# Optimization experiments

Measured on AMD Instinct MI355X. Metric: run time of the kernel, lower is better.

## Reference

```python
import jax, jax.numpy as jnp
import numpy as np

GROUP_SIZES = [5, 5, 5, 5, 5, 5, 4]  # 7 concept groups, sum = 34
LN_EPS = 1e-5


def setup_inputs() -> dict:
    key = jax.random.key(0)
    ks = jax.random.split(key, 12)
    B, N, D, K, P, C, NC, H = 256, 196, 768, 7, 512, 34, 7, 3072
    img_feat_map = jax.random.normal(ks[0], (B, N, D), dtype=jnp.float32)
    # torch: Embedding weight uniform in [-1/K, 1/K]
    vq_codebook = (jax.random.uniform(ks[1], (K, D), dtype=jnp.float32) * 2.0 - 1.0) / K
    agg_codebook = jax.random.normal(ks[2], (K, D), dtype=jnp.float32)
    W1 = jax.random.normal(ks[3], (D, H), dtype=jnp.float32) * 0.02
    b1 = jnp.zeros((H,), dtype=jnp.float32)
    W2 = jax.random.normal(ks[4], (H, D), dtype=jnp.float32) * 0.02
    b2 = jnp.zeros((D,), dtype=jnp.float32)
    ln_gamma = jnp.ones((D,), dtype=jnp.float32)
    ln_beta = jnp.zeros((D,), dtype=jnp.float32)
    W_proj = jax.random.normal(ks[5], (D, P), dtype=jnp.float32) * 0.02
    concept_emb = jax.random.normal(ks[6], (C, P), dtype=jnp.float32)
    concept_emb = concept_emb / jnp.linalg.norm(concept_emb, axis=-1, keepdims=True)
    cls_W = jax.random.normal(ks[7], (C, NC), dtype=jnp.float32) * 0.02
    cls_b = jnp.zeros((NC,), dtype=jnp.float32)
    logit_scale = jnp.float32(100.0)  # detached CLIP logit scale
    return {
        "img_feat_map": img_feat_map, "vq_codebook": vq_codebook,
        "agg_codebook": agg_codebook, "W1": W1, "b1": b1, "W2": W2, "b2": b2,
        "ln_gamma": ln_gamma, "ln_beta": ln_beta, "W_proj": W_proj,
        "concept_emb": concept_emb, "cls_W": cls_W, "cls_b": cls_b,
        "logit_scale": logit_scale,
    }


def _pairwise_sq_dists(x, cb):
    # x: [B, N, D], cb: [K, D] -> [B, N, K]
    x_sq = jnp.sum(x * x, axis=-1, keepdims=True)           # [B, N, 1]
    cb_sq = jnp.sum(cb * cb, axis=-1)                        # [K]
    dot = jnp.einsum("bnd,kd->bnk", x, cb)                  # [B, N, K]
    return x_sq + cb_sq - 2.0 * dot


def _avg_effective_rank(x, threshold=0.99):
    # x: [B, N, D]; per-sample SVD, rank = #{cumsum(S)/sum(S) <= thr}
    S = jnp.linalg.svd(jax.lax.stop_gradient(x), compute_uv=False)  # [B, min(N,D)]
    energy = jnp.cumsum(S, axis=-1) / jnp.sum(S, axis=-1, keepdims=True)
    ranks = jnp.sum(energy <= threshold, axis=-1)
    return jnp.mean(ranks.astype(jnp.float32))


def reference(img_feat_map, vq_codebook, agg_codebook, W1, b1, W2, b2,
              ln_gamma, ln_beta, W_proj, concept_emb, cls_W, cls_b, logit_scale):
    x = img_feat_map  # [B, N, D]

    avg_rank = _avg_effective_rank(x)

    # --- VectorQuantizeAggregator: soft assignment to 7 codes ---
    d_agg = _pairwise_sq_dists(x, agg_codebook)              # [B, N, K]
    soft = jax.nn.softmax(-d_agg, axis=-1)                   # [B, N, K]
    agg = jnp.einsum("bnk,bnd->bkd", soft, x)               # [B, K, D]

    # --- VectorQuantizer: hard argmin + gather (one-hot @ codebook) ---
    d_vq = _pairwise_sq_dists(x, vq_codebook)                # [B, N, K]
    idx = jnp.argmin(d_vq, axis=-1)                          # [B, N] int
    quantized = vq_codebook[idx]                             # [B, N, D] gather == onehot @ cb
    sg = jax.lax.stop_gradient
    codebook_loss = jnp.mean((quantized - sg(x)) ** 2)
    commitment_loss = jnp.mean((sg(quantized) - x) ** 2)
    vq_loss = codebook_loss + 1.0 * commitment_loss

    # --- bridge: FFN -> LayerNorm -> proj -> L2 normalize ---
    h = jax.nn.gelu(agg @ W1 + b1, approximate=False) @ W2 + b2  # [B, K, D]
    mu = jnp.mean(h, axis=-1, keepdims=True)
    var = jnp.mean((h - mu) ** 2, axis=-1, keepdims=True)
    hn = (h - mu) * jax.lax.rsqrt(var + LN_EPS) * ln_gamma + ln_beta
    tok = hn @ W_proj                                        # [B, K, 512]
    tok = tok / jnp.linalg.norm(tok, axis=-1, keepdims=True)

    # --- per-group concept logits: token g vs its concept slice ---
    logits_list = []
    start = 0
    for g, sz in enumerate(GROUP_SIZES):
        ce = concept_emb[start:start + sz]                   # [sz, 512]
        logits_list.append(logit_scale * (tok[:, g, :] @ ce.T))  # [B, sz]
        start += sz
    image_logits = jnp.concatenate(logits_list, axis=-1)     # [B, 34]

    cls_logits = image_logits @ cls_W + cls_b                # [B, 7]
    return (cls_logits, image_logits, vq_loss, avg_rank)
```

## Files before the change

### kernel.cpp

```cpp
#include <hip/hip_runtime.h>
#include <hip/hip_bf16.h>
#include <math.h>

using hbf = __hip_bfloat16;
typedef __bf16 bf16x8 __attribute__((ext_vector_type(8)));
typedef float f32x4 __attribute__((ext_vector_type(4)));

__device__ inline float r16d(float v){
  int x;
  x = __builtin_bit_cast(int, v);
  v += __builtin_bit_cast(float, __builtin_amdgcn_mov_dpp(x, 0x121, 0xf, 0xf, true));
  x = __builtin_bit_cast(int, v);
  v += __builtin_bit_cast(float, __builtin_amdgcn_mov_dpp(x, 0x122, 0xf, 0xf, true));
  x = __builtin_bit_cast(int, v);
  v += __builtin_bit_cast(float, __builtin_amdgcn_mov_dpp(x, 0x124, 0xf, 0xf, true));
  x = __builtin_bit_cast(int, v);
  v += __builtin_bit_cast(float, __builtin_amdgcn_mov_dpp(x, 0x128, 0xf, 0xf, true));
  return v;
}
__device__ inline void r16d4(float& a, float& b, float& c, float& d){
#define R16STAGE(ctl) { \
  int xa=__builtin_bit_cast(int,a), xb=__builtin_bit_cast(int,b); \
  int xc=__builtin_bit_cast(int,c), xd=__builtin_bit_cast(int,d); \
  a += __builtin_bit_cast(float, __builtin_amdgcn_mov_dpp(xa, ctl, 0xf, 0xf, true)); \
// ... 99 lines not shown
    }
    cx0 = nx0; cx1 = nx1; cx2 = nx2;
  }
  __syncthreads();
  for (int i = tid; i < 5376; i += 512) cA[i] = 0.f;
  __syncthreads();
  for (int w = 0; w < 8; ++w){
    if (wave == w){
#pragma unroll
      for (int k = 0; k < 7; ++k)
#pragma unroll
        for (int c = 0; c < 3; ++c){
          float* p = &cA[k*768 + c*256 + (lane<<2)];
          p[0] += aR[k][c].x; p[1] += aR[k][c].y; p[2] += aR[k][c].z; p[3] += aR[k][c].w;
        }
    }
    __syncthreads();
  }
  for (int i = tid; i < 5376; i += 512) aggbf[(size_t)b*5376 + i] = __float2bfloat16(cA[i]);
  if (lane == 0) atomicAdd(&scal[0], loss);
}

__global__ __launch_bounds__(512) void k_gram(const float* __restrict__ x, float* __restrict__ G){
  __shared__ hbf Xs[208*104];
  const int tid = threadIdx.x, lane = tid & 63, wave = tid >> 6;
  const int b = blockIdx.x;
  const int l15 = lane & 15;
  const int fr0 = wave, fr1 = wave + 8;
  const bool f1 = (fr1 < 13);
  f32x4 acc0[13] = {};
  f32x4 acc1[13] = {};
  const float* xb = x + (size_t)b*196*768;
  for (int kc = 0; kc < 8; ++kc){
    __syncthreads();
    for (int u = tid; u < 4992; u += 512){
      const int r = u / 24, c4 = u - r*24;
      ushort4 val;
      if (r < 196){
        float4 f = *(const float4*)(xb + (size_t)r*768 + kc*96 + c4*4);
        hbf t0 = __float2bfloat16(f.x), t1 = __float2bfloat16(f.y);
        hbf t2 = __float2bfloat16(f.z), t3 = __float2bfloat16(f.w);
        val.x = *(const unsigned short*)&t0; val.y = *(const unsigned short*)&t1;
        val.z = *(const unsigned short*)&t2; val.w = *(const unsigned short*)&t3;
      } else { val.x = 0; val.y = 0; val.z = 0; val.w = 0; }
      *(ushort4*)&Xs[r*104 + c4*4] = val;
    }
    __syncthreads();
#pragma unroll
    for (int kk = 0; kk < 3; ++kk){
      const int ko = kk*32 + (lane>>4)*8;
      bf16x8 a0 = *(const bf16x8*)&Xs[(fr0*16 + l15)*104 + ko];
      bf16x8 a1 = f1 ? *(const bf16x8*)&Xs[(fr1*16 + l15)*104 + ko] : a0;
#pragma unroll
      for (int fc = 0; fc < 13; ++fc){
        bf16x8 bb = *(const bf16x8*)&Xs[(fc*16 + l15)*104 + ko];
        acc0[fc] = __builtin_amdgcn_mfma_f32_16x16x32_bf16(a0, bb, acc0[fc], 0, 0, 0);
        if (f1) acc1[fc] = __builtin_amdgcn_mfma_f32_16x16x32_bf16(a1, bb, acc1[fc], 0, 0, 0);
      }
    }
  }
  const size_t gb = (size_t)b*38416;
  const int cr = (lane>>4)*4;
#pragma unroll
  for (int fc = 0; fc < 13; ++fc){
    const int gc = fc*16 + l15;
    if (gc < 196){
#pragma unroll
      for (int r = 0; r < 4; ++r){
        const int gr = fr0*16 + cr + r;
        if (gr < 196) G[gb + (size_t)gr*196 + gc] = acc0[fc][r];
      }
      if (f1){
#pragma unroll
        for (int r = 0; r < 4; ++r){
          const int gr = fr1*16 + cr + r;
          if (gr < 196) G[gb + (size_t)gr*196 + gc] = acc1[fc][r];
        }
      }
    }
  }
}

#define ESTR 196
#define FOLD4(vv4) { vv4.x = (oc==0)? v0 : vv4.x; vv4.y = (oc==1)? v0 : vv4.y; \
                     vv4.z = (oc==2)? v0 : vv4.z; vv4.w = (oc==3)? v0 : vv4.w; }
#define VHOIST(colc, out) { \
  const int col_ = (colc) + jc4; \
  const float4 xv_ = *(const float4*)(rowk + col_); \
  float4 vp_; \
  if (col_ > base){ vp_ = xv_; } \
  else if (col_ + 3 <= base){ vp_ = make_float4(0.f,0.f,0.f,0.f); } \
  else { vp_.x = 0.f; \
         vp_.y = (col_+1 > base) ? xv_.y : 0.f; \
         vp_.z = (col_+2 > base) ? xv_.z : 0.f; \
         vp_.w = xv_.w; } \
  out = vp_; sig += vp_.x*vp_.x + vp_.y*vp_.y + vp_.z*vp_.z + vp_.w*vp_.w; }

__global__ __launch_bounds__(1024) void k_eigen(const float* __restrict__ G, float* __restrict__ scal){
  extern __shared__ float S[];
  float* A   = S;
  float* ww  = S + 38496;
  float* dd  = S + 38752;
  float* ee  = S + 38952;
  float* e2  = S + 39152;
  float* red2= S + 39352;
  const int n = 196;
  const int tid = threadIdx.x, lane = tid & 63, wave = tid >> 6;
  const int grp = lane >> 4, c16 = lane & 15;
  const int jc4 = c16 << 2;
  const int rbase = (wave << 2) + grp;
  const int b = blockIdx.x;
  {
    const float4* Gv = (const float4*)(G + (size_t)b*38416);
    float4* Av = (float4*)A;
    for (int u = tid; u < 9604; u += 1024) Av[u] = Gv[u];
    if (tid < 80) S[38416 + tid] = 0.f;
    if (tid < 256) ww[tid] = 0.f;
  }
  __syncthreads();
  for (int k = 0; k <= 130; ++k){
    const int base = k + 1, m = n - 1 - k;
    const float* rowk = &A[(size_t)k*ESTR];
    const float x0 = rowk[base];
    if (tid == 0) ww[k] = 0.f;
    float4 v4_0, v4_1, v4_2, v4_3;
    float sig = 0.f;
    VHOIST(0,   v4_0)
    VHOIST(64,  v4_1)
    VHOIST(128, v4_2)
    {
      float4 vp_ = make_float4(0.f,0.f,0.f,0.f);
      if (c16 == 0){
        vp_ = *(const float4*)(rowk + 192);
        sig += vp_.x*vp_.x + vp_.y*vp_.y + vp_.z*vp_.z + vp_.w*vp_.w;
      }
      v4_3 = vp_;
    }
    sig = r16d(sig);
    float tau = 0.f, v0 = 0.f, alpha = x0;
    if (sig > 1e-20f){
      const float mu = sqrtf(x0*x0 + sig);
      alpha = (x0 > 0.f) ? -mu : mu;
      v0 = x0 - alpha;
      tau = 2.f/(sig + v0*v0);
    }
    if (tid == 0) ee[k] = alpha;
    if (c16 == ((base >> 2) & 15)){
      const int oc = base & 3;
      const int op = base >> 6;
      if (op == 0){ FOLD4(v4_0) } else if (op == 1){ FOLD4(v4_1) } else { FOLD4(v4_2) }
    }
    const int p0 = base >> 6;
    const int i0 = rbase, i1 = 64 + rbase, i2 = 128 + rbase, i3 = 192 + rbase;
    float vr_0=0.f, vr_1=0.f, vr_2=0.f, vr_3=0.f;
    float wr_0=0.f, wr_1=0.f, wr_2=0.f, wr_3=0.f;
    if (tau != 0.f){
      float a0c=0.f, a1c=0.f, a2c=0.f, a3c=0.f;
#define MV_T(IV, ACC) { \
      if (IV < m){ \
        const float* Ar = &A[(size_t)(base+IV)*ESTR]; \
        if (0 >= p0){ ACC += d4(*(const float4*)(Ar + jc4),       v4_0); } \
        if (1 >= p0){ ACC += d4(*(const float4*)(Ar + 64 + jc4),  v4_1); } \
        if (2 >= p0){ ACC += d4(*(const float4*)(Ar + 128 + jc4), v4_2); } \
        if (c16 == 0){ ACC += d4(*(const float4*)(Ar + 192), v4_3); } } }
      MV_T(i0, a0c)
      MV_T(i1, a1c)
      MV_T(i2, a2c)
      MV_T(i3, a3c)
#undef MV_T
      r16d4(a0c, a1c, a2c, a3c);
      float cpart = 0.f;
      {
        wr_0 = tau*a0c;
        vr_0 = (i0 == 0) ? v0 : rowk[base+i0];
        cpart += vr_0*wr_0;
        if (c16 == 0) ww[base+i0] = wr_0;
      }
      if (i1 < m){
        wr_1 = tau*a1c; vr_1 = rowk[base+i1];
        cpart += vr_1*wr_1;
        if (c16 == 0) ww[base+i1] = wr_1;
      }
      if (i2 < m){
        wr_2 = tau*a2c; vr_2 = rowk[base+i2];
        cpart += vr_2*wr_2;
        if (c16 == 0) ww[base+i2] = wr_2;
      }
      if (i3 < m){
        wr_3 = tau*a3c; vr_3 = rowk[base+i3];
        cpart += vr_3*wr_3;
        if (c16 == 0) ww[base+i3] = wr_3;
      }
      cpart += __shfl_xor(cpart, 16);
      cpart += __shfl_xor(cpart, 32);
      if (lane == 0) red2[wave] = cpart;
    }
    __syncthreads();
    if (tau != 0.f){
      const float4* r2 = (const float4*)red2;
      const float4 q0 = r2[0], q1 = r2[1], q2 = r2[2], q3 = r2[3];
      const float vtw = (q0.x+q0.y+q0.z+q0.w) + (q1.x+q1.y+q1.z+q1.w)
                      + (q2.x+q2.y+q2.z+q2.w) + (q3.x+q3.y+q3.z+q3.w);
      const float c2 = 0.5f*tau*vtw;
      float4 w4_0, w4_1, w4_2, w4_3 = make_float4(0.f,0.f,0.f,0.f);
      { const float4 t4 = *(const float4*)(ww + jc4);
        w4_0.x = t4.x - c2*v4_0.x; w4_0.y = t4.y - c2*v4_0.y; w4_0.z = t4.z - c2*v4_0.z; w4_0.w = t4.w - c2*v4_0.w; }
      { const float4 t4 = *(const float4*)(ww + 64 + jc4);
        w4_1.x = t4.x - c2*v4_1.x; w4_1.y = t4.y - c2*v4_1.y; w4_1.z = t4.z - c2*v4_1.z; w4_1.w = t4.w - c2*v4_1.w; }
      { const float4 t4 = *(const float4*)(ww + 128 + jc4);
        w4_2.x = t4.x - c2*v4_2.x; w4_2.y = t4.y - c2*v4_2.y; w4_2.z = t4.z - c2*v4_2.z; w4_2.w = t4.w - c2*v4_2.w; }
      if (c16 == 0){
        const float4 t4 = *(const float4*)(ww + 192);
        w4_3.x = t4.x - c2*v4_3.x; w4_3.y = t4.y - c2*v4_3.y; w4_3.z = t4.z - c2*v4_3.z; w4_3.w = t4.w - c2*v4_3.w; }
#define UP_T(IV, VRV, WRV) { \
      if (IV < m){ \
        const float vi = VRV; \
        const float wi = WRV - c2*vi; \
        float* Ar = &A[(size_t)(base+IV)*ESTR]; \
        if (0 >= p0){ float4 a = *(const float4*)(Ar + jc4); \
          a.x -= vi*w4_0.x + wi*v4_0.x; a.y -= vi*w4_0.y + wi*v4_0.y; \
          a.z -= vi*w4_0.z + wi*v4_0.z; a.w -= vi*w4_0.w + wi*v4_0.w; \
          *(float4*)(Ar + jc4) = a; } \
        if (1 >= p0){ float4 a = *(const float4*)(Ar + 64 + jc4); \
          a.x -= vi*w4_1.x + wi*v4_1.x; a.y -= vi*w4_1.y + wi*v4_1.y; \
          a.z -= vi*w4_1.z + wi*v4_1.z; a.w -= vi*w4_1.w + wi*v4_1.w; \
          *(float4*)(Ar + 64 + jc4) = a; } \
        if (2 >= p0){ float4 a = *(const float4*)(Ar + 128 + jc4); \
          a.x -= vi*w4_2.x + wi*v4_2.x; a.y -= vi*w4_2.y + wi*v4_2.y; \
          a.z -= vi*w4_2.z + wi*v4_2.z; a.w -= vi*w4_2.w + wi*v4_2.w; \
          *(float4*)(Ar + 128 + jc4) = a; } \
        if (c16 == 0){ float4 a = *(const float4*)(Ar + 192); \
          a.x -= vi*w4_3.x + wi*v4_3.x; a.y -= vi*w4_3.y + wi*v4_3.y; \
          a.z -= vi*w4_3.z + wi*v4_3.z; a.w -= vi*w4_3.w + wi*v4_3.w; \
          *(float4*)(Ar + 192) = a; } } }
      UP_T(i0, vr_0, wr_0)
      UP_T(i1, vr_1, wr_1)
      UP_T(i2, vr_2, wr_2)
      UP_T(i3, vr_3, wr_3)
#undef UP_T
    }
    __syncthreads();
  }
  if (wave == 0){
    float vrT[16], wrT[16];
    for (int k = 131; k <= n-3; ++k){
      const int base = k + 1, m = n - 1 - k;
      const float* rowk = &A[(size_t)k*ESTR];
      const float x0 = rowk[base];
      if (lane == 0) ww[k] = 0.f;
      float4 v4_2, v4_3;
      float sig = 0.f;
      VHOIST(128, v4_2)
      {
        float4 vp_ = make_float4(0.f,0.f,0.f,0.f);
        if (c16 == 0){
          const float4 xv_ = *(const float4*)(rowk + 192);
          if (192 > base){ vp_ = xv_; }
          else { vp_.x = 0.f;
                 vp_.y = (193 > base) ? xv_.y : 0.f;
                 vp_.z = (194 > base) ? xv_.z : 0.f;
                 vp_.w = xv_.w; }
        }
        v4_3 = vp_; sig += vp_.x*vp_.x + vp_.y*vp_.y + vp_.z*vp_.z + vp_.w*vp_.w;
      }
      sig = r16d(sig);
      float tau = 0.f, v0 = 0.f, alpha = x0;
      if (sig > 1e-20f){
        const float mu = sqrtf(x0*x0 + sig);
        alpha = (x0 > 0.f) ? -mu : mu;
        v0 = x0 - alpha;
        tau = 2.f/(sig + v0*v0);
      }
      if (lane == 0) ee[k] = alpha;
      if (c16 == ((base >> 2) & 15)){
        const int oc = base & 3;
        if ((base >> 6) == 2){ FOLD4(v4_2) } else { FOLD4(v4_3) }
      }
      if (tau != 0.f){
        float cpart = 0.f;
#pragma unroll
        for (int t = 0; t < 16; ++t){
          const int i_ = (t << 2) + grp;
          float vrv = 0.f, wrv = 0.f;
          if (i_ < m){
            const float* Ar = &A[(size_t)(base+i_)*ESTR];
            float acc = d4(*(const float4*)(Ar + 128 + jc4), v4_2);
            if (c16 == 0) acc += d4(*(const float4*)(Ar + 192), v4_3);
            acc = r16d(acc);
            wrv = tau*acc;
            vrv = (i_ == 0) ? v0 : rowk[base+i_];
            cpart += vrv*wrv;
            if (c16 == 0) ww[base+i_] = wrv;
          }
          vrT[t] = vrv; wrT[t] = wrv;
        }
        cpart += __shfl_xor(cpart, 16);
        cpart += __shfl_xor(cpart, 32);
        const float c2 = 0.5f*tau*cpart;
        __threadfence_block();
        float4 w4_2, w4_3 = make_float4(0.f,0.f,0.f,0.f);
        { const float4 t4 = *(const float4*)(ww + 128 + jc4);
          w4_2.x = t4.x - c2*v4_2.x; w4_2.y = t4.y - c2*v4_2.y; w4_2.z = t4.z - c2*v4_2.z; w4_2.w = t4.w - c2*v4_2.w; }
        if (c16 == 0){
          const float4 t4 = *(const float4*)(ww + 192);
          w4_3.x = t4.x - c2*v4_3.x; w4_3.y = t4.y - c2*v4_3.y; w4_3.z = t4.z - c2*v4_3.z; w4_3.w = t4.w - c2*v4_3.w; }
#pragma unroll
        for (int t = 0; t < 16; ++t){
          const int i_ = (t << 2) + grp;
          if (i_ < m){
            const float vi = vrT[t];
            const float wi = wrT[t] - c2*vi;
            float* Ar = &A[(size_t)(base+i_)*ESTR];
            float4 a = *(const float4*)(Ar + 128 + jc4);
            a.x -= vi*w4_2.x + wi*v4_2.x; a.y -= vi*w4_2.y + wi*v4_2.y;
            a.z -= vi*w4_2.z + wi*v4_2.z; a.w -= vi*w4_2.w + wi*v4_2.w;
            *(float4*)(Ar + 128 + jc4) = a;
            if (c16 == 0){
              float4 a3 = *(const float4*)(Ar + 192);
              a3.x -= vi*w4_3.x + wi*v4_3.x; a3.y -= vi*w4_3.y + wi*v4_3.y;
              a3.z -= vi*w4_3.z + wi*v4_3.z; a3.w -= vi*w4_3.w + wi*v4_3.w;
              *(float4*)(Ar + 192) = a3;
            }
          }
        }
        __threadfence_block();
      }
    }
  }
  __syncthreads();
  if (tid < n) dd[tid] = A[(size_t)tid*ESTR + tid];
  if (tid == 0) ee[n-2] = A[(size_t)(n-1)*ESTR + (n-2)];
  __syncthreads();
  if (tid < n-1) e2[tid] = ee[tid]*ee[tid];
  __syncthreads();
  float lo = 1e30f, hi = -1e30f;
  if (tid < n){
    const float rr = ((tid > 0) ? fabsf(ee[tid-1]) : 0.f) + ((tid < n-1) ? fabsf(ee[tid]) : 0.f);
    lo = dd[tid] - rr; hi = dd[tid] + rr;
  }
  {
    float l2 = lo, h2 = hi;
#pragma unroll
    for (int o = 32; o > 0; o >>= 1){
      l2 = fminf(l2, __shfl_xor(l2, o));
      h2 = fmaxf(h2, __shfl_xor(h2, o));
    }
    if (lane == 0){ ww[wave] = l2; red2[wave] = h2; }
  }
  __syncthreads();
  float glo = ww[0], ghi = red2[0];
#pragma unroll
  for (int w2 = 1; w2 < 16; ++w2){ glo = fminf(glo, ww[w2]); ghi = fmaxf(ghi, red2[w2]); }
  __syncthreads();
  float sv = 0.f;
  if (tid < n){
    float lob = glo, hib = ghi;
    for (int it2 = 0; it2 < 18; ++it2){
      const float mid = 0.5f*(lob + hib);
      float q = dd[0] - mid;
      int cnt = (q < 0.f) ? 1 : 0;
      for (int i = 1; i < n; ++i){
        const float r = fast_rcp(q);
        q = (dd[i] - mid) - e2[i-1]*r;
        q = (fabsf(q) < 1e-6f) ? -1e-6f : q;
        cnt += (q < 0.f) ? 1 : 0;
      }
      if (cnt <= tid) lob = mid; else hib = mid;
    }
    sv = sqrtf(fmaxf(0.5f*(lob + hib), 0.f));
  }
  __syncthreads();
  if (tid < n) ww[tid] = sv;
  __syncthreads();
  if (tid == 0){
    float tot = 0.f;
    for (int i = 0; i < n; ++i) tot += ww[i];
    const float thr = 0.99f*tot;
    float cs = 0.f; int rank = 0;
    for (int i = n-1; i >= 0; --i){ cs += ww[i]; rank += (cs <= thr) ? 1 : 0; }
    atomicAdd(&scal[1], (float)rank);
  }
}

__global__ __launch_bounds__(256) void k_tr(const float* __restrict__ in, hbf* __restrict__ outp,
                                            int Rr, int Cc){
  __shared__ float t[32][33];
  const int tid = threadIdx.x;
  const int lc = tid & 31, lr = tid >> 5;
  const int c0 = blockIdx.x*32, r0 = blockIdx.y*32;
#pragma unroll
  for (int i = 0; i < 4; ++i)
    t[lr + i*8][lc] = in[(size_t)(r0 + lr + i*8)*Cc + c0 + lc];
  __syncthreads();
#pragma unroll
  for (int i = 0; i < 4; ++i)
    outp[(size_t)(c0 + lr + i*8)*Rr + r0 + lc] = __float2bfloat16(t[lc][lr + i*8]);
}

template<int EPI>
__global__ __launch_bounds__(512) void k_gemm128(const hbf* __restrict__ Aa, const hbf* __restrict__ Bb,
    const float* __restrict__ bias, void* __restrict__ outp, int Ni, int Ki){
  __shared__ hbf As[128*72];
  __shared__ hbf Bs[128*72];
  const int tid = threadIdx.x, lane = tid & 63, wave = tid >> 6;
  const int row0 = blockIdx.y*128, col0 = blockIdx.x*128;
  const int m0 = (wave >> 2)*64, n0 = (wave & 3)*32;
  const int l15 = lane & 15, lk = (lane >> 4)*8;
  const int sr = tid >> 3, sc = (tid & 7)*8;
  f32x4 acc[4][2] = {};
  for (int kt = 0; kt < Ki; kt += 64){
    __syncthreads();
    *(uint4*)&As[sr*72 + sc]      = *(const uint4*)&Aa[(size_t)(row0+sr)*Ki + kt + sc];
    *(uint4*)&As[(sr+64)*72 + sc] = *(const uint4*)&Aa[(size_t)(row0+sr+64)*Ki + kt + sc];
    *(uint4*)&Bs[sr*72 + sc]      = *(const uint4*)&Bb[(size_t)(col0+sr)*Ki + kt + sc];
    *(uint4*)&Bs[(sr+64)*72 + sc] = *(const uint4*)&Bb[(size_t)(col0+sr+64)*Ki + kt + sc];
    __syncthreads();
#pragma unroll
    for (int kk = 0; kk < 2; ++kk){
      const int ko = kk*32 + lk;
      bf16x8 b0 = *(const bf16x8*)&Bs[(n0 + l15)*72 + ko];
      bf16x8 b1 = *(const bf16x8*)&Bs[(n0 + 16 + l15)*72 + ko];
#pragma unroll
      for (int mi = 0; mi < 4; ++mi){
        bf16x8 a = *(const bf16x8*)&As[(m0 + mi*16 + l15)*72 + ko];
        acc[mi][0] = __builtin_amdgcn_mfma_f32_16x16x32_bf16(a, b0, acc[mi][0], 0, 0, 0);
        acc[mi][1] = __builtin_amdgcn_mfma_f32_16x16x32_bf16(a, b1, acc[mi][1], 0, 0, 0);
      }
    }
  }
  const int cr = (lane >> 4)*4;
#pragma unroll
  for (int mi = 0; mi < 4; ++mi){
#pragma unroll
    for (int ni = 0; ni < 2; ++ni){
      const int gcol = col0 + n0 + ni*16 + l15;
#pragma unroll
      for (int r = 0; r < 4; ++r){
        const int grow = row0 + m0 + mi*16 + cr + r;
        float v = acc[mi][ni][r];
        if (EPI == 1){
          v += bias[gcol];
          v = 0.5f*v*(1.f + erff(v*0.70710678118654752f));
          ((hbf*)outp)[(size_t)grow*Ni + gcol] = __float2bfloat16(v);
        } else if (EPI == 2){
          v += bias[gcol];
          ((float*)outp)[(size_t)grow*Ni + gcol] = v;
        } else {
          ((float*)outp)[(size_t)grow*Ni + gcol] = v;
        }
      }
    }
  }
}

template<int EPI>
__global__ __launch_bounds__(256) void k_gemm(const hbf* __restrict__ Aa, const hbf* __restrict__ Bb,
    const float* __restrict__ bias, void* __restrict__ outp, int Mi, int Ni, int Ki){
  __shared__ hbf As[64*72];
  __shared__ hbf Bs[64*72];
  const int tid = threadIdx.x, lane = tid & 63, wave = tid >> 6;
  const int row0 = blockIdx.y*64, col0 = blockIdx.x*64;
  const int m0 = (wave >> 1)*32, n0 = (wave & 1)*32;
// ... 84 lines not shown
__global__ __launch_bounds__(256) void k_head(const float* __restrict__ tok, const float* __restrict__ ce,
    const float* __restrict__ clsW, const float* __restrict__ clsb, const float* __restrict__ lgs,
    float* __restrict__ out){
  __shared__ float tkn[7*512];
  __shared__ float il[40];
  const int tid = threadIdx.x, lane = tid & 63, wave = tid >> 6;
  const int b = blockIdx.x;
  const float ls = lgs[0];
  for (int g = wave; g < 7; g += 4){
    const float* tr = tok + (size_t)(b*7 + g)*512;
    float4 u0 = *(const float4*)(tr + (lane<<3));
    float4 u1 = *(const float4*)(tr + (lane<<3) + 4);
    float s = d4(u0,u0) + d4(u1,u1);
    s = wred(s);
    const float inv = 1.f/sqrtf(s);
    float* dst = &tkn[g*512 + (lane<<3)];
    dst[0] = u0.x*inv; dst[1] = u0.y*inv; dst[2] = u0.z*inv; dst[3] = u0.w*inv;
    dst[4] = u1.x*inv; dst[5] = u1.y*inv; dst[6] = u1.z*inv; dst[7] = u1.w*inv;
  }
  __syncthreads();
  for (int c = wave; c < 34; c += 4){
    const int g = (c < 30) ? (c/5) : 6;
    const float* tp = &tkn[g*512 + (lane<<3)];
    const float* cp = ce + (size_t)c*512 + (lane<<3);
    float s = tp[0]*cp[0] + tp[1]*cp[1] + tp[2]*cp[2] + tp[3]*cp[3]
            + tp[4]*cp[4] + tp[5]*cp[5] + tp[6]*cp[6] + tp[7]*cp[7];
    s = wred(s);
    if (lane == 0){
      const float v = ls*s;
      il[c] = v;
      out[1792 + b*34 + c] = v;
    }
  }
  __syncthreads();
  if (tid < 7){
    float s = clsb[tid];
    for (int c = 0; c < 34; ++c) s += il[c]*clsW[c*7 + tid];
    out[b*7 + tid] = s;
  }
}

__global__ void k_fin(const float* __restrict__ scal, float* __restrict__ out){
  if (threadIdx.x == 0){
    out[10496] = 2.f*scal[0]/(float)(256*196*768);
    out[10497] = scal[1]*(1.f/256.f);
  }
}

extern "C" void kernel_launch(void* const* d_in, const int* in_sizes, int n_in,
                              void* d_out, int out_size, void* d_ws, size_t ws_size,
                              hipStream_t stream) {
  (void)in_sizes; (void)n_in; (void)out_size; (void)ws_size;
  const float* x    = (const float*)d_in[0];
  const float* vqcb = (const float*)d_in[1];
  const float* agcb = (const float*)d_in[2];
  const float* W1   = (const float*)d_in[3];
  const float* b1   = (const float*)d_in[4];
  const float* W2   = (const float*)d_in[5];
  const float* b2   = (const float*)d_in[6];
  const float* gam  = (const float*)d_in[7];
  const float* bet  = (const float*)d_in[8];
  const float* Wp   = (const float*)d_in[9];
  const float* ce   = (const float*)d_in[10];
  const float* clsW = (const float*)d_in[11];
  const float* clsb = (const float*)d_in[12];
  const float* lgs  = (const float*)d_in[13];
  float* out = (float*)d_out;
  char* w = (char*)d_ws;

  float* scal  = (float*)w;
  float* G     = (float*)(w + 256);
  hbf*   aggbf = (hbf*)(w + 39338240ULL);
  hbf*   W1t   = (hbf*)(w + 42090752ULL);
  hbf*   W2t   = (hbf*)(w + 46809344ULL);
  hbf*   Wpt   = (hbf*)(w + 51527936ULL);
  hbf*   h1    = (hbf*)(w + 256);
  float* hbuf  = (float*)(w + 256 + 16777216ULL);
  hbf*   hn    = (hbf*)(w + 256 + 25165824ULL);
  float* tok   = (float*)(w + 256 + 29360128ULL);

  k_init<<<dim3(1), dim3(64), 0, stream>>>(scal);
  k_dist<<<dim3(256), dim3(512), 0, stream>>>(x, vqcb, agcb, aggbf, scal);
  k_gram<<<dim3(256), dim3(512), 0, stream>>>(x, G);
  const int EIG_SMEM = 39368*4;
  hipFuncSetAttribute((const void*)k_eigen, hipFuncAttributeMaxDynamicSharedMemorySize, EIG_SMEM);
  k_eigen<<<dim3(256), dim3(1024), EIG_SMEM, stream>>>(G, scal);
  k_tr<<<dim3(96,24), dim3(256), 0, stream>>>(W1, W1t, 768, 3072);
  k_tr<<<dim3(24,96), dim3(256), 0, stream>>>(W2, W2t, 3072, 768);
  k_tr<<<dim3(16,24), dim3(256), 0, stream>>>(Wp, Wpt, 768, 512);
  k_gemm128<1><<<dim3(24,14), dim3(512), 0, stream>>>(aggbf, W1t, b1, (void*)h1, 3072, 768);
  k_gemm<2><<<dim3(12,28), dim3(256), 0, stream>>>(h1, W2t, b2, (void*)hbuf, 1792, 768, 3072);
  k_ln<<<dim3(448), dim3(256), 0, stream>>>(hbuf, gam, bet, hn);
  k_gemm<3><<<dim3(8,28), dim3(256), 0, stream>>>(hn, Wpt, nullptr, (void*)tok, 1792, 512, 768);
  k_head<<<dim3(256), dim3(256), 0, stream>>>(tok, ce, clsW, clsb, lgs, out);
  k_fin<<<dim3(1), dim3(64), 0, stream>>>(scal, out);
}
```

Before: 1.034 ms.

## Block Householder tridiagonalization two reflectors per step in eigen kernel

Restructures the Householder tridiagonalization in k_eigen so each iteration computes two reflectors and applies a combined rank-4 update to the shared-memory matrix. The second reflector's vector and matvec are derived on the fly from the first update without materializing the intermediate matrix. This halves the number of full matrix read-modify-write passes and the associated block barriers per reflector pair. In exchange it adds extra reductions and register pressure, and the serial single-wave tail now starts one step later.

```diff
diff --git a/kernel.cpp b/kernel.cpp
--- a/kernel.cpp
+++ b/kernel.cpp
@@ -205,28 +205,30 @@
 }
 
 #define ESTR 196
-#define FOLD4(vv4) { vv4.x = (oc==0)? v0 : vv4.x; vv4.y = (oc==1)? v0 : vv4.y; \
-                     vv4.z = (oc==2)? v0 : vv4.z; vv4.w = (oc==3)? v0 : vv4.w; }
-#define VHOIST(colc, out) { \
-  const int col_ = (colc) + jc4; \
+#define FOLD4v(FR, V0) { FR.x = (oc==0)? (V0) : FR.x; FR.y = (oc==1)? (V0) : FR.y; \
+                         FR.z = (oc==2)? (V0) : FR.z; FR.w = (oc==3)? (V0) : FR.w; }
+#define VH(COLC, BASE, OUT) { \
+  const int col_ = (COLC) + jc4; \
   const float4 xv_ = *(const float4*)(rowk + col_); \
   float4 vp_; \
-  if (col_ > base){ vp_ = xv_; } \
-  else if (col_ + 3 <= base){ vp_ = make_float4(0.f,0.f,0.f,0.f); } \
+  if (col_ > (BASE)){ vp_ = xv_; } \
+  else if (col_ + 3 <= (BASE)){ vp_ = make_float4(0.f,0.f,0.f,0.f); } \
   else { vp_.x = 0.f; \
-         vp_.y = (col_+1 > base) ? xv_.y : 0.f; \
-         vp_.z = (col_+2 > base) ? xv_.z : 0.f; \
+         vp_.y = (col_+1 > (BASE)) ? xv_.y : 0.f; \
+         vp_.z = (col_+2 > (BASE)) ? xv_.z : 0.f; \
          vp_.w = xv_.w; } \
-  out = vp_; sig += vp_.x*vp_.x + vp_.y*vp_.y + vp_.z*vp_.z + vp_.w*vp_.w; }
+  OUT = vp_; sig += vp_.x*vp_.x + vp_.y*vp_.y + vp_.z*vp_.z + vp_.w*vp_.w; }
 
 __global__ __launch_bounds__(1024) void k_eigen(const float* __restrict__ G, float* __restrict__ scal){
   extern __shared__ float S[];
-  float* A   = S;
-  float* ww  = S + 38496;
-  float* dd  = S + 38752;
-  float* ee  = S + 38952;
-  float* e2  = S + 39152;
-  float* red2= S + 39352;
+  float* A    = S;
+  float* ww1  = S + 38496;
+  float* ww2  = S + 38752;
+  float* dd   = S + 39008;
+  float* ee   = S + 39208;
+  float* e2   = S + 39408;
+  float* red2 = S + 39608;
+  float* red2b= S + 39624;
   const int n = 196;
   const int tid = threadIdx.x, lane = tid & 63, wave = tid >> 6;
   const int grp = lane >> 4, c16 = lane & 15;
@@ -237,143 +239,247 @@
     const float4* Gv = (const float4*)(G + (size_t)b*38416);
     float4* Av = (float4*)A;
     for (int u = tid; u < 9604; u += 1024) Av[u] = Gv[u];
-    if (tid < 80) S[38416 + tid] = 0.f;
-    if (tid < 256) ww[tid] = 0.f;
-  }
-  __syncthreads();
-  for (int k = 0; k <= 130; ++k){
-    const int base = k + 1, m = n - 1 - k;
-    const float* rowk = &A[(size_t)k*ESTR];
-    const float x0 = rowk[base];
-    if (tid == 0) ww[k] = 0.f;
-    float4 v4_0, v4_1, v4_2, v4_3;
+    if (tid < 592) S[38416 + tid] = 0.f;
+  }
+  __syncthreads();
+  for (int k = 0; k <= 130; k += 2){
+    const int base1 = k + 1, base2 = k + 2;
+    const int m1 = n - 1 - k, m2 = n - 2 - k;
+    const float* rowk  = &A[(size_t)k*ESTR];
+    const float* rowk1 = &A[(size_t)base1*ESTR];
+    if (tid == 0 && k > 0){
+      ww1[k-1] = 0.f; ww1[k] = 0.f;
+      ww2[k]   = 0.f; ww2[k+1] = 0.f;
+    }
+    const float x01 = rowk[base1];
+    float4 v1f0, v1f1, v1f2, v1f3;
     float sig = 0.f;
-    VHOIST(0,   v4_0)
-    VHOIST(64,  v4_1)
-    VHOIST(128, v4_2)
+    VH(0,   base1, v1f0)
+    VH(64,  base1, v1f1)
+    VH(128, base1, v1f2)
+    { float4 vp = make_float4(0.f,0.f,0.f,0.f);
+      if (c16 == 0){ vp = *(const float4*)(rowk + 192);
+        sig += vp.x*vp.x + vp.y*vp.y + vp.z*vp.z + vp.w*vp.w; }
+      v1f3 = vp; }
+    sig = r16d(sig);
+    float tau1 = 0.f, v01 = 0.f, alpha1 = x01;
+    if (sig > 1e-20f){
+      const float mu = sqrtf(x01*x01 + sig);
+      alpha1 = (x01 > 0.f) ? -mu : mu;
+      v01 = x01 - alpha1;
+      tau1 = 2.f/(sig + v01*v01);
+    }
+    if (tid == 0) ee[k] = alpha1;
+    if (c16 == ((base1 >> 2) & 15)){
+      const int oc = base1 & 3, op = base1 >> 6;
+      if (op == 0){ FOLD4v(v1f0, v01) } else if (op == 1){ FOLD4v(v1f1, v01) } else { FOLD4v(v1f2, v01) }
+    }
+    const int p0 = base1 >> 6;
+    const int i0r = rbase, i1r = 64 + rbase, i2r = 128 + rbase, i3r = 192 + rbase;
     {
-      float4 vp_ = make_float4(0.f,0.f,0.f,0.f);
-      if (c16 == 0){
-        vp_ = *(const float4*)(rowk + 192);
-        sig += vp_.x*vp_.x + vp_.y*vp_.y + vp_.z*vp_.z + vp_.w*vp_.w;
-      }
-      v4_3 = vp_;
-    }
-    sig = r16d(sig);
-    float tau = 0.f, v0 = 0.f, alpha = x0;
-    if (sig > 1e-20f){
-      const float mu = sqrtf(x0*x0 + sig);
-      alpha = (x0 > 0.f) ? -mu : mu;
-      v0 = x0 - alpha;
-      tau = 2.f/(sig + v0*v0);
-    }
-    if (tid == 0) ee[k] = alpha;
-    if (c16 == ((base >> 2) & 15)){
-      const int oc = base & 3;
-      const int op = base >> 6;
-      if (op == 0){ FOLD4(v4_0) } else if (op == 1){ FOLD4(v4_1) } else { FOLD4(v4_2) }
-    }
-    const int p0 = base >> 6;
-    const int i0 = rbase, i1 = 64 + rbase, i2 = 128 + rbase, i3 = 192 + rbase;
-    float vr_0=0.f, vr_1=0.f, vr_2=0.f, vr_3=0.f;
-    float wr_0=0.f, wr_1=0.f, wr_2=0.f, wr_3=0.f;
-    if (tau != 0.f){
-      float a0c=0.f, a1c=0.f, a2c=0.f, a3c=0.f;
-#define MV_T(IV, ACC) { \
-      if (IV < m){ \
-        const float* Ar = &A[(size_t)(base+IV)*ESTR]; \
-        if (0 >= p0){ ACC += d4(*(const float4*)(Ar + jc4),       v4_0); } \
-        if (1 >= p0){ ACC += d4(*(const float4*)(Ar + 64 + jc4),  v4_1); } \
-        if (2 >= p0){ ACC += d4(*(const float4*)(Ar + 128 + jc4), v4_2); } \
-        if (c16 == 0){ ACC += d4(*(const float4*)(Ar + 192), v4_3); } } }
-      MV_T(i0, a0c)
-      MV_T(i1, a1c)
-      MV_T(i2, a2c)
-      MV_T(i3, a3c)
-#undef MV_T
+      float a0c = 0.f, a1c = 0.f, a2c = 0.f, a3c = 0.f;
+#define MV1(IV, ACC) { \
+      if ((IV) < m1){ \
+        const float* Ar = &A[(size_t)(base1+(IV))*ESTR]; \
+        if (0 >= p0) ACC += d4(*(const float4*)(Ar + jc4), v1f0); \
+        if (1 >= p0) ACC += d4(*(const float4*)(Ar + 64 + jc4), v1f1); \
+        if (2 >= p0) ACC += d4(*(const float4*)(Ar + 128 + jc4), v1f2); \
+        if (c16 == 0) ACC += d4(*(const float4*)(Ar + 192), v1f3); } }
+      MV1(i0r, a0c) MV1(i1r, a1c) MV1(i2r, a2c) MV1(i3r, a3c)
+#undef MV1
       r16d4(a0c, a1c, a2c, a3c);
-      float cpart = 0.f;
-      {
-        wr_0 = tau*a0c;
-        vr_0 = (i0 == 0) ? v0 : rowk[base+i0];
-        cpart += vr_0*wr_0;
-        if (c16 == 0) ww[base+i0] = wr_0;
-      }
-      if (i1 < m){
-        wr_1 = tau*a1c; vr_1 = rowk[base+i1];
-        cpart += vr_1*wr_1;
-        if (c16 == 0) ww[base+i1] = wr_1;
-      }
-      if (i2 < m){
-        wr_2 = tau*a2c; vr_2 = rowk[base+i2];
-        cpart += vr_2*wr_2;
-        if (c16 == 0) ww[base+i2] = wr_2;
-      }
-      if (i3 < m){
-        wr_3 = tau*a3c; vr_3 = rowk[base+i3];
-        cpart += vr_3*wr_3;
-        if (c16 == 0) ww[base+i3] = wr_3;
-      }
-      cpart += __shfl_xor(cpart, 16);
-      cpart += __shfl_xor(cpart, 32);
-      if (lane == 0) red2[wave] = cpart;
-    }
-    __syncthreads();
-    if (tau != 0.f){
+      float cp = 0.f;
+#define CP1(IV, ACC) { \
+      if ((IV) < m1){ \
+        const float wr_ = tau1*(ACC); \
+        const float vr_ = ((IV) == 0) ? v01 : rowk[base1+(IV)]; \
+        cp += vr_*wr_; \
+        if (c16 == 0) ww1[base1+(IV)] = wr_; } }
+      CP1(i0r, a0c) CP1(i1r, a1c) CP1(i2r, a2c) CP1(i3r, a3c)
+#undef CP1
+      cp += __shfl_xor(cp, 16);
+      cp += __shfl_xor(cp, 32);
+      if (lane == 0) red2[wave] = cp;
+    }
+    __syncthreads();
+    float c21, w1head, tau2 = 0.f, v02 = 0.f;
+    float4 w1f0, w1f1, w1f2, w1f3;
+    float4 v2f0, v2f1, v2f2, v2f3;
+    {
       const float4* r2 = (const float4*)red2;
       const float4 q0 = r2[0], q1 = r2[1], q2 = r2[2], q3 = r2[3];
       const float vtw = (q0.x+q0.y+q0.z+q0.w) + (q1.x+q1.y+q1.z+q1.w)
                       + (q2.x+q2.y+q2.z+q2.w) + (q3.x+q3.y+q3.z+q3.w);
-      const float c2 = 0.5f*tau*vtw;
-      float4 w4_0, w4_1, w4_2, w4_3 = make_float4(0.f,0.f,0.f,0.f);
-      { const float4 t4 = *(const float4*)(ww + jc4);
-        w4_0.x = t4.x - c2*v4_0.x; w4_0.y = t4.y - c2*v4_0.y; w4_0.z = t4.z - c2*v4_0.z; w4_0.w = t4.w - c2*v4_0.w; }
-      { const float4 t4 = *(const float4*)(ww + 64 + jc4);
-        w4_1.x = t4.x - c2*v4_1.x; w4_1.y = t4.y - c2*v4_1.y; w4_1.z = t4.z - c2*v4_1.z; w4_1.w = t4.w - c2*v4_1.w; }
-      { const float4 t4 = *(const float4*)(ww + 128 + jc4);
-        w4_2.x = t4.x - c2*v4_2.x; w4_2.y = t4.y - c2*v4_2.y; w4_2.z = t4.z - c2*v4_2.z; w4_2.w = t4.w - c2*v4_2.w; }
-      if (c16 == 0){
-        const float4 t4 = *(const float4*)(ww + 192);
-        w4_3.x = t4.x - c2*v4_3.x; w4_3.y = t4.y - c2*v4_3.y; w4_3.z = t4.z - c2*v4_3.z; w4_3.w = t4.w - c2*v4_3.w; }
-#define UP_T(IV, VRV, WRV) { \
-      if (IV < m){ \
-        const float vi = VRV; \
-        const float wi = WRV - c2*vi; \
-        float* Ar = &A[(size_t)(base+IV)*ESTR]; \
+      c21 = 0.5f*tau1*vtw;
+      w1head = ww1[base1] - c21*v01;
+      if (tid == 0) A[(size_t)base1*ESTR + base1] = rowk1[base1] - 2.f*v01*w1head;
+#define W1F(COLC, VF, OUT) { \
+      const float4 t4 = *(const float4*)(ww1 + (COLC) + jc4); \
+      OUT.x = t4.x - c21*VF.x; OUT.y = t4.y - c21*VF.y; \
+      OUT.z = t4.z - c21*VF.z; OUT.w = t4.w - c21*VF.w; }
+      W1F(0,   v1f0, w1f0)
+      W1F(64,  v1f1, w1f1)
+      W1F(128, v1f2, w1f2)
+      { float4 wp = make_float4(0.f,0.f,0.f,0.f);
+        if (c16 == 0){ const float4 t4 = *(const float4*)(ww1 + 192);
+          wp.x = t4.x - c21*v1f3.x; wp.y = t4.y - c21*v1f3.y;
+          wp.z = t4.z - c21*v1f3.z; wp.w = t4.w - c21*v1f3.w; }
+        w1f3 = wp; }
+#undef W1F
+      float sig2 = 0.f;
+#define V2F(COLC, VF1, WF1, OUT) { \
+      const int col_ = (COLC) + jc4; \
+      const float4 r1_ = *(const float4*)(rowk1 + col_); \
+      float4 rp_; \
+      rp_.x = r1_.x - v01*WF1.x - w1head*VF1.x; \
+      rp_.y = r1_.y - v01*WF1.y - w1head*VF1.y; \
+      rp_.z = r1_.z - v01*WF1.z - w1head*VF1.z; \
+      rp_.w = r1_.w - v01*WF1.w - w1head*VF1.w; \
+      float4 vp_; \
+      if (col_ > base2){ vp_ = rp_; } \
+      else if (col_ + 3 <= base2){ vp_ = make_float4(0.f,0.f,0.f,0.f); } \
+      else { vp_.x = 0.f; \
+             vp_.y = (col_+1 > base2) ? rp_.y : 0.f; \
+             vp_.z = (col_+2 > base2) ? rp_.z : 0.f; \
+             vp_.w = rp_.w; } \
+      OUT = vp_; sig2 += vp_.x*vp_.x + vp_.y*vp_.y + vp_.z*vp_.z + vp_.w*vp_.w; }
+      V2F(0,   v1f0, w1f0, v2f0)
+      V2F(64,  v1f1, w1f1, v2f1)
+      V2F(128, v1f2, w1f2, v2f2)
+      { float4 vp = make_float4(0.f,0.f,0.f,0.f);
+        if (c16 == 0){ const float4 r1_ = *(const float4*)(rowk1 + 192);
+          vp.x = r1_.x - v01*w1f3.x - w1head*v1f3.x;
+          vp.y = r1_.y - v01*w1f3.y - w1head*v1f3.y;
+          vp.z = r1_.z - v01*w1f3.z - w1head*v1f3.z;
+          vp.w = r1_.w - v01*w1f3.w - w1head*v1f3.w;
+          sig2 += vp.x*vp.x + vp.y*vp.y + vp.z*vp.z + vp.w*vp.w; }
+        v2f3 = vp; }
+#undef V2F
+      sig2 = r16d(sig2);
+      const float vb2 = rowk[base2];
+      const float w1b2 = ww1[base2] - c21*vb2;
+      const float x02 = rowk1[base2] - v01*w1b2 - w1head*vb2;
+      float alpha2 = x02;
+      if (sig2 > 1e-20f){
+        const float mu = sqrtf(x02*x02 + sig2);
+        alpha2 = (x02 > 0.f) ? -mu : mu;
+        v02 = x02 - alpha2;
+        tau2 = 2.f/(sig2 + v02*v02);
+      }
+      if (tid == 0) ee[base1] = alpha2;
+      if (c16 == ((base2 >> 2) & 15)){
+        const int oc = base2 & 3, op = base2 >> 6;
+        if (op == 0){ FOLD4v(v2f0, v02) } else if (op == 1){ FOLD4v(v2f1, v02) } else { FOLD4v(v2f2, v02) }
+      }
+      float swv = d4(w1f0,v2f0) + d4(w1f1,v2f1) + d4(w1f2,v2f2) + d4(w1f3,v2f3);
+      float svv = d4(v1f0,v2f0) + d4(v1f1,v2f1) + d4(v1f2,v2f2) + d4(v1f3,v2f3);
+      swv = r16d(swv); svv = r16d(svv);
+      float a0c = 0.f, a1c = 0.f, a2c = 0.f, a3c = 0.f;
+#define MV2(IV, ACC) { \
+      if ((IV) < m2){ \
+        const float* Ar = &A[(size_t)(base2+(IV))*ESTR]; \
+        if (0 >= p0) ACC += d4(*(const float4*)(Ar + jc4), v2f0); \
+        if (1 >= p0) ACC += d4(*(const float4*)(Ar + 64 + jc4), v2f1); \
+        if (2 >= p0) ACC += d4(*(const float4*)(Ar + 128 + jc4), v2f2); \
+        if (c16 == 0) ACC += d4(*(const float4*)(Ar + 192), v2f3); } }
+      MV2(i0r, a0c) MV2(i1r, a1c) MV2(i2r, a2c) MV2(i3r, a3c)
+#undef MV2
+      r16d4(a0c, a1c, a2c, a3c);
+      float cp = 0.f;
+#define CP2(IV, ACC) { \
+      if ((IV) < m2){ \
+        const int r_ = base2 + (IV); \
+        const float v1r_ = rowk[r_]; \
+        const float w1r_ = ww1[r_] - c21*v1r_; \
+        const float u2_ = (ACC) - v1r_*swv - w1r_*svv; \
+        const float w2r_ = tau2*u2_; \
+        const float v2r_ = (r_ == base2) ? v02 : (rowk1[r_] - v01*w1r_ - w1head*v1r_); \
+        cp += v2r_*w2r_; \
+        if (c16 == 0) ww2[r_] = w2r_; } }
+      CP2(i0r, a0c) CP2(i1r, a1c) CP2(i2r, a2c) CP2(i3r, a3c)
+#undef CP2
+      cp += __shfl_xor(cp, 16);
+      cp += __shfl_xor(cp, 32);
+      if (lane == 0) red2b[wave] = cp;
+    }
+    __syncthreads();
+    {
+      const float4* r2 = (const float4*)red2b;
+      const float4 q0 = r2[0], q1 = r2[1], q2 = r2[2], q3 = r2[3];
+      const float vtw2 = (q0.x+q0.y+q0.z+q0.w) + (q1.x+q1.y+q1.z+q1.w)
+                       + (q2.x+q2.y+q2.z+q2.w) + (q3.x+q3.y+q3.z+q3.w);
+      const float c22 = 0.5f*tau2*vtw2;
+      float4 w2f0, w2f1, w2f2, w2f3;
+#define W2F(COLC, VF, OUT) { \
+      const float4 t4 = *(const float4*)(ww2 + (COLC) + jc4); \
+      OUT.x = t4.x - c22*VF.x; OUT.y = t4.y - c22*VF.y; \
+      OUT.z = t4.z - c22*VF.z; OUT.w = t4.w - c22*VF.w; }
+      W2F(0,   v2f0, w2f0)
+      W2F(64,  v2f1, w2f1)
+      W2F(128, v2f2, w2f2)
+      { float4 wp = make_float4(0.f,0.f,0.f,0.f);
+        if (c16 == 0){ const float4 t4 = *(const float4*)(ww2 + 192);
+          wp.x = t4.x - c22*v2f3.x; wp.y = t4.y - c22*v2f3.y;
+          wp.z = t4.z - c22*v2f3.z; wp.w = t4.w - c22*v2f3.w; }
+        w2f3 = wp; }
+#undef W2F
+#define UPD(IV) { \
+      if ((IV) < m2){ \
+        const int r_ = base2 + (IV); \
+        const float v1r = rowk[r_]; \
+        const float w1r = ww1[r_] - c21*v1r; \
+        const float v2r = (r_ == base2) ? v02 : (rowk1[r_] - v01*w1r - w1head*v1r); \
+        const float w2r = ww2[r_] - c22*v2r; \
+        float* Ar = &A[(size_t)r_*ESTR]; \
         if (0 >= p0){ float4 a = *(const float4*)(Ar + jc4); \
-          a.x -= vi*w4_0.x + wi*v4_0.x; a.y -= vi*w4_0.y + wi*v4_0.y; \
-          a.z -= vi*w4_0.z + wi*v4_0.z; a.w -= vi*w4_0.w + wi*v4_0.w; \
+          a.x -= v1r*w1f0.x + w1r*v1f0.x + v2r*w2f0.x + w2r*v2f0.x; \
+          a.y -= v1r*w1f0.y + w1r*v1f0.y + v2r*w2f0.y + w2r*v2f0.y; \
+          a.z -= v1r*w1f0.z + w1r*v1f0.z + v2r*w2f0.z + w2r*v2f0.z; \
+          a.w -= v1r*w1f0.w + w1r*v1f0.w + v2r*w2f0.w + w2r*v2f0.w; \
           *(float4*)(Ar + jc4) = a; } \
         if (1 >= p0){ float4 a = *(const float4*)(Ar + 64 + jc4); \
-          a.x -= vi*w4_1.x + wi*v4_1.x; a.y -= vi*w4_1.y + wi*v4_1.y; \
-          a.z -= vi*w4_1.z + wi*v4_1.z; a.w -= vi*w4_1.w + wi*v4_1.w; \
+          a.x -= v1r*w1f1.x + w1r*v1f1.x + v2r*w2f1.x + w2r*v2f1.x; \
+          a.y -= v1r*w1f1.y + w1r*v1f1.y + v2r*w2f1.y + w2r*v2f1.y; \
+          a.z -= v1r*w1f1.z + w1r*v1f1.z + v2r*w2f1.z + w2r*v2f1.z; \
+          a.w -= v1r*w1f1.w + w1r*v1f1.w + v2r*w2f1.w + w2r*v2f1.w; \
           *(float4*)(Ar + 64 + jc4) = a; } \
         if (2 >= p0){ float4 a = *(const float4*)(Ar + 128 + jc4); \
-          a.x -= vi*w4_2.x + wi*v4_2.x; a.y -= vi*w4_2.y + wi*v4_2.y; \
-          a.z -= vi*w4_2.z + wi*v4_2.z; a.w -= vi*w4_2.w + wi*v4_2.w; \
+          a.x -= v1r*w1f2.x + w1r*v1f2.x + v2r*w2f2.x + w2r*v2f2.x; \
+          a.y -= v1r*w1f2.y + w1r*v1f2.y + v2r*w2f2.y + w2r*v2f2.y; \
+          a.z -= v1r*w1f2.z + w1r*v1f2.z + v2r*w2f2.z + w2r*v2f2.z; \
+          a.w -= v1r*w1f2.w + w1r*v1f2.w + v2r*w2f2.w + w2r*v2f2.w; \
           *(float4*)(Ar + 128 + jc4) = a; } \
         if (c16 == 0){ float4 a = *(const float4*)(Ar + 192); \
-          a.x -= vi*w4_3.x + wi*v4_3.x; a.y -= vi*w4_3.y + wi*v4_3.y; \
-          a.z -= vi*w4_3.z + wi*v4_3.z; a.w -= vi*w4_3.w + wi*v4_3.w; \
+          a.x -= v1r*w1f3.x + w1r*v1f3.x + v2r*w2f3.x + w2r*v2f3.x; \
+          a.y -= v1r*w1f3.y + w1r*v1f3.y + v2r*w2f3.y + w2r*v2f3.y; \
+          a.z -= v1r*w1f3.z + w1r*v1f3.z + v2r*w2f3.z + w2r*v2f3.z; \
+          a.w -= v1r*w1f3.w + w1r*v1f3.w + v2r*w2f3.w + w2r*v2f3.w; \
           *(float4*)(Ar + 192) = a; } } }
-      UP_T(i0, vr_0, wr_0)
-      UP_T(i1, vr_1, wr_1)
-      UP_T(i2, vr_2, wr_2)
-      UP_T(i3, vr_3, wr_3)
-#undef UP_T
+      UPD(i0r) UPD(i1r) UPD(i2r) UPD(i3r)
+#undef UPD
     }
     __syncthreads();
   }
   if (wave == 0){
+    float* ww = ww1;
     float vrT[16], wrT[16];
-    for (int k = 131; k <= n-3; ++k){
+    for (int k = 132; k <= n-3; ++k){
       const int base = k + 1, m = n - 1 - k;
       const float* rowk = &A[(size_t)k*ESTR];
-      const float x0 = rowk[base];
-      if (lane == 0) ww[k] = 0.f;
+      const float x01 = rowk[base];
+      if (lane == 0){ ww[k] = 0.f; ww[k-1] = 0.f; }
       float4 v4_2, v4_3;
       float sig = 0.f;
-      VHOIST(128, v4_2)
+      { const int col_ = 128 + jc4;
+        const float4 xv_ = *(const float4*)(rowk + col_);
+        float4 vp_;
+        if (col_ > base){ vp_ = xv_; }
+        else if (col_ + 3 <= base){ vp_ = make_float4(0.f,0.f,0.f,0.f); }
+        else { vp_.x = 0.f;
+               vp_.y = (col_+1 > base) ? xv_.y : 0.f;
+               vp_.z = (col_+2 > base) ? xv_.z : 0.f;
+               vp_.w = xv_.w; }
+        v4_2 = vp_; sig += vp_.x*vp_.x + vp_.y*vp_.y + vp_.z*vp_.z + vp_.w*vp_.w; }
       {
         float4 vp_ = make_float4(0.f,0.f,0.f,0.f);
         if (c16 == 0){
@@ -387,17 +493,17 @@
         v4_3 = vp_; sig += vp_.x*vp_.x + vp_.y*vp_.y + vp_.z*vp_.z + vp_.w*vp_.w;
       }
       sig = r16d(sig);
-      float tau = 0.f, v0 = 0.f, alpha = x0;
+      float tau = 0.f, v0 = 0.f, alpha = x01;
       if (sig > 1e-20f){
-        const float mu = sqrtf(x0*x0 + sig);
-        alpha = (x0 > 0.f) ? -mu : mu;
-        v0 = x0 - alpha;
+        const float mu = sqrtf(x01*x01 + sig);
+        alpha = (x01 > 0.f) ? -mu : mu;
+        v0 = x01 - alpha;
         tau = 2.f/(sig + v0*v0);
       }
       if (lane == 0) ee[k] = alpha;
       if (c16 == ((base >> 2) & 15)){
         const int oc = base & 3;
-        if ((base >> 6) == 2){ FOLD4(v4_2) } else { FOLD4(v4_3) }
+        if ((base >> 6) == 2){ FOLD4v(v4_2, v0) } else { FOLD4v(v4_3, v0) }
       }
       if (tau != 0.f){
         float cpart = 0.f;
@@ -468,12 +574,12 @@
       l2 = fminf(l2, __shfl_xor(l2, o));
       h2 = fmaxf(h2, __shfl_xor(h2, o));
     }
-    if (lane == 0){ ww[wave] = l2; red2[wave] = h2; }
-  }
-  __syncthreads();
-  float glo = ww[0], ghi = red2[0];
-#pragma unroll
-  for (int w2 = 1; w2 < 16; ++w2){ glo = fminf(glo, ww[w2]); ghi = fmaxf(ghi, red2[w2]); }
+    if (lane == 0){ ww1[wave] = l2; red2[wave] = h2; }
+  }
+  __syncthreads();
+  float glo = ww1[0], ghi = red2[0];
+#pragma unroll
+  for (int w2 = 1; w2 < 16; ++w2){ glo = fminf(glo, ww1[w2]); ghi = fmaxf(ghi, red2[w2]); }
   __syncthreads();
   float sv = 0.f;
   if (tid < n){
@@ -493,14 +599,14 @@
     sv = sqrtf(fmaxf(0.5f*(lob + hib), 0.f));
   }
   __syncthreads();
-  if (tid < n) ww[tid] = sv;
+  if (tid < n) ww1[tid] = sv;
   __syncthreads();
   if (tid == 0){
     float tot = 0.f;
-    for (int i = 0; i < n; ++i) tot += ww[i];
+    for (int i = 0; i < n; ++i) tot += ww1[i];
     const float thr = 0.99f*tot;
     float cs = 0.f; int rank = 0;
-    for (int i = n-1; i >= 0; --i){ cs += ww[i]; rank += (cs <= thr) ? 1 : 0; }
+    for (int i = n-1; i >= 0; --i){ cs += ww1[i]; rank += (cs <= thr) ? 1 : 0; }
     atomicAdd(&scal[1], (float)rank);
   }
 }
@@ -751,7 +857,7 @@
   k_init<<<dim3(1), dim3(64), 0, stream>>>(scal);
   k_dist<<<dim3(256), dim3(512), 0, stream>>>(x, vqcb, agcb, aggbf, scal);
   k_gram<<<dim3(256), dim3(512), 0, stream>>>(x, G);
-  const int EIG_SMEM = 39368*4;
+  const int EIG_SMEM = 39640*4;
   hipFuncSetAttribute((const void*)k_eigen, hipFuncAttributeMaxDynamicSharedMemorySize, EIG_SMEM);
   k_eigen<<<dim3(256), dim3(1024), EIG_SMEM, stream>>>(G, scal);
   k_tr<<<dim3(96,24), dim3(256), 0, stream>>>(W1, W1t, 768, 3072);
```

New measurement: 1.017 ms. Within noise of the previous version (-1.6%).
